# Kernel tuning notes

Hardware: AMD Instinct MI355X
Metric: run time of the kernel (lower is better)

## Reference

```python
import jax, jax.numpy as jnp
import numpy as np

RADIUS = 0.2
NSAMPLE = 32


def ball_query(new_xyz, xyz, radius, nsample):
    # new_xyz: (B, M, 3), xyz: (B, N, 3) -> idx: (B, M, nsample) int32
    B, M, _ = new_xyz.shape
    N = xyz.shape[1]
    # pairwise squared distances (B, M, N)
    diff = new_xyz[:, :, None, :] - xyz[:, None, :, :]
    dist2 = jnp.sum(diff * diff, axis=-1)
    mask = dist2 < (radius * radius)
    ar = jnp.arange(N, dtype=jnp.int32)
    masked = jnp.where(mask, ar[None, None, :], jnp.int32(N + 1))  # (B,M,N)
    sorted_idx = jnp.sort(masked, axis=2)[:, :, :nsample]          # (B,M,nsample)
    invalid = sorted_idx >= N
    first = sorted_idx[:, :, 0:1]
    idx = jnp.where(invalid, jnp.broadcast_to(first, sorted_idx.shape), sorted_idx)
    return idx


def group_points(points, idx):
    # points: (B, C, N), idx: (B, M, nsample) -> (B, C, M, nsample)
    B, C, N = points.shape
    M, ns = idx.shape[1], idx.shape[2]
    flat = jnp.broadcast_to(idx.reshape(B, 1, M * ns), (B, C, M * ns))
    return jnp.take_along_axis(points, flat, axis=2).reshape(B, C, M, ns)


def setup_inputs() -> dict:
    key = jax.random.key(0)
    k1, k2, k3 = jax.random.split(key, 3)
    xyz = jax.random.uniform(k1, (8, 16384, 3), dtype=jnp.float32)
    new_xyz = jax.random.uniform(k2, (8, 1024, 3), dtype=jnp.float32)
    features = jax.random.normal(k3, (8, 64, 16384), dtype=jnp.float32)
    return {"xyz": xyz, "new_xyz": new_xyz, "features": features}


def reference(xyz, new_xyz, features):
    idx = ball_query(new_xyz, xyz, RADIUS, NSAMPLE)          # (B,M,ns)
    xyz_t = jnp.transpose(xyz, (0, 2, 1))                    # (B,3,N)
    grouped_xyz = group_points(xyz_t, idx)                   # (B,3,M,ns)
    grouped_xyz = grouped_xyz - jnp.transpose(new_xyz, (0, 2, 1))[:, :, :, None]
    grouped_features = group_points(features, idx)           # (B,C,M,ns)
    new_features = jnp.concatenate([grouped_xyz, grouped_features], axis=1)
    return new_features                                      # (B, 3+C, M, ns)
```

## Files before the change

kernel.cpp:

```cpp
#include <hip/hip_runtime.h>


#define N_PTS   16384
#define M_Q     1024
#define B_SZ    8
#define NSAMP   32
#define NCH     64
#define R2      0.04f
#define OUT_CH  (3 + NCH)

__global__ __launch_bounds__(256) void transpose_kernel(
    const float* __restrict__ feat, float* __restrict__ ft)
{
    __shared__ float tile[64][65];
    const int b   = blockIdx.x >> 8;
    const int n0  = (blockIdx.x & 255) << 6;
    const int tid = threadIdx.x;
    const float* __restrict__ fb = feat + (size_t)b * NCH * N_PTS;
    float* __restrict__ tb       = ft   + ((size_t)b * N_PTS + n0) * NCH;

#pragma unroll
    for (int j = 0; j < 16; ++j) {
        const int idx = j * 256 + tid;
        const int c = idx >> 6, nn = idx & 63;
        tile[c][nn] = fb[(size_t)c * N_PTS + n0 + nn];
    }
    __syncthreads();
#pragma unroll
    for (int j = 0; j < 16; ++j) {
        const int idx = j * 256 + tid;
        const int nn = idx >> 6, cc = idx & 63;
        tb[(size_t)nn * NCH + cc] = tile[cc][nn];
    }
}

__global__ __launch_bounds__(128) void qg_main(
    const float* __restrict__ xyz,
    const float* __restrict__ new_xyz,
    const float* __restrict__ ft,
    float* __restrict__ out)
{
    const int tid  = threadIdx.x;
    const int w    = tid >> 6;
    const int lane = tid & 63;
    const int q    = blockIdx.x * 2 + w;
    const int b    = q >> 10;
    const int m    = q & (M_Q - 1);

    __shared__ int   idx_sh[2][NSAMP];
    __shared__ float tile[2][32][33];

    const float cx = new_xyz[q * 3 + 0];
    const float cy = new_xyz[q * 3 + 1];
    const float cz = new_xyz[q * 3 + 2];
    const float* __restrict__ xb = xyz + (size_t)b * N_PTS * 3;

    const unsigned long long lmask = (1ull << lane) - 1ull;
    int cnt = 0;
    for (int base = 0; base < N_PTS && cnt < NSAMP; base += 128) {
        const int nA = base + lane;
        const int nB = base + 64 + lane;
        const float ax = xb[nA * 3 + 0], ay = xb[nA * 3 + 1], az = xb[nA * 3 + 2];
        const float bx = xb[nB * 3 + 0], by = xb[nB * 3 + 1], bz = xb[nB * 3 + 2];

        {
            const float dx = __fsub_rn(cx, ax), dy = __fsub_rn(cy, ay), dz = __fsub_rn(cz, az);
            const float d2 = __fadd_rn(__fadd_rn(__fmul_rn(dx, dx), __fmul_rn(dy, dy)),
                                       __fmul_rn(dz, dz));
            const bool hit = d2 < R2;
            const unsigned long long mk = __ballot(hit);
            if (hit) {
                const int slot = cnt + __popcll(mk & lmask);
                if (slot < NSAMP) idx_sh[w][slot] = nA;
            }
            cnt += (int)__popcll(mk);
        }
        {
            const float dx = __fsub_rn(cx, bx), dy = __fsub_rn(cy, by), dz = __fsub_rn(cz, bz);
            const float d2 = __fadd_rn(__fadd_rn(__fmul_rn(dx, dx), __fmul_rn(dy, dy)),
                                       __fmul_rn(dz, dz));
            const bool hit = d2 < R2;
            const unsigned long long mk = __ballot(hit);
            if (hit) {
                const int slot = cnt + __popcll(mk & lmask);
                if (slot < NSAMP) idx_sh[w][slot] = nB;
            }
            cnt += (int)__popcll(mk);
        }
    }
    __syncthreads();

    if (lane < NSAMP) {
        const int v0 = (cnt > 0) ? idx_sh[w][0] : 0;
        if (lane >= cnt) idx_sh[w][lane] = v0;
    }
    __syncthreads();

    float* __restrict__ ob = out + ((size_t)b * OUT_CH * M_Q + (size_t)m) * NSAMP;
    for (int e = lane; e < 3 * NSAMP; e += 64) {
        const int c = e >> 5, s = e & 31;
        const int n = idx_sh[w][s];
        const float ctr = (c == 0) ? cx : ((c == 1) ? cy : cz);
        ob[(size_t)c * (M_Q * NSAMP) + s] = __fsub_rn(xb[n * 3 + c], ctr);
    }

    const float* __restrict__ ftb = ft + (size_t)b * N_PTS * NCH;
    const int sgrp = lane >> 3;
    const int c4   = lane & 7;

    for (int chunk = 0; chunk < 2; ++chunk) {
        float4 vals[4];
#pragma unroll
        for (int i = 0; i < 4; ++i) {
            const int s = i * 8 + sgrp;
            const int n = idx_sh[w][s];
            const float4* row = (const float4*)(ftb + (size_t)n * NCH + chunk * 32);
            vals[i] = row[c4];
        }
        __syncthreads();
#pragma unroll
        for (int i = 0; i < 4; ++i) {
            const int s = i * 8 + sgrp;
            tile[w][c4 * 4 + 0][s] = vals[i].x;
            tile[w][c4 * 4 + 1][s] = vals[i].y;
            tile[w][c4 * 4 + 2][s] = vals[i].z;
            tile[w][c4 * 4 + 3][s] = vals[i].w;
        }
        __syncthreads();
#pragma unroll
        for (int j = 0; j < 16; ++j) {
            const int idx = j * 64 + lane;
            const int c_local = idx >> 5;
            const int s = idx & 31;
            ob[(size_t)(3 + chunk * 32 + c_local) * (M_Q * NSAMP) + s] =
                tile[w][c_local][s];
        }
    }
}

__global__ __launch_bounds__(256) void qg_fallback(
    const float* __restrict__ xyz, const float* __restrict__ new_xyz,
    const float* __restrict__ feat, float* __restrict__ out)
{
    const int tid  = threadIdx.x;
    const int w    = tid >> 6;
    const int lane = tid & 63;
    const int q    = blockIdx.x * 4 + w;
    const int b    = q >> 10;
    const int m    = q & (M_Q - 1);

    __shared__ int idx_sh[4][NSAMP];

    const float cx = new_xyz[q * 3 + 0];
    const float cy = new_xyz[q * 3 + 1];
    const float cz = new_xyz[q * 3 + 2];
    const float* __restrict__ xb = xyz + (size_t)b * N_PTS * 3;

    int cnt = 0;
    for (int base = 0; base < N_PTS && cnt < NSAMP; base += 64) {
        const int n = base + lane;
        const float dx = __fsub_rn(cx, xb[n * 3 + 0]);
        const float dy = __fsub_rn(cy, xb[n * 3 + 1]);
        const float dz = __fsub_rn(cz, xb[n * 3 + 2]);
        const float d2 = __fadd_rn(__fadd_rn(__fmul_rn(dx, dx), __fmul_rn(dy, dy)),
                                   __fmul_rn(dz, dz));
        const bool hit = d2 < R2;
        const unsigned long long mk = __ballot(hit);
        if (hit) {
            const int slot = cnt + __popcll(mk & ((1ull << lane) - 1ull));
            if (slot < NSAMP) idx_sh[w][slot] = n;
        }
        cnt += (int)__popcll(mk);
    }
    __syncthreads();
    if (lane < NSAMP) {
        const int v0 = (cnt > 0) ? idx_sh[w][0] : 0;
        if (lane >= cnt) idx_sh[w][lane] = v0;
    }
    __syncthreads();

    const float* __restrict__ fb = feat + (size_t)b * NCH * N_PTS;
    float* __restrict__ ob = out + ((size_t)b * OUT_CH * M_Q + (size_t)m) * NSAMP;
    for (int e = lane; e < OUT_CH * NSAMP; e += 64) {
        const int c = e >> 5, s = e & 31;
        const int n = idx_sh[w][s];
        float v;
        if (c < 3) {
            const float ctr = (c == 0) ? cx : ((c == 1) ? cy : cz);
            v = __fsub_rn(xb[n * 3 + c], ctr);
        } else {
            v = fb[(size_t)(c - 3) * N_PTS + n];
        }
        ob[(size_t)c * (M_Q * NSAMP) + s] = v;
    }
}

extern "C" void kernel_launch(void* const* d_in, const int* in_sizes, int n_in,
                              void* d_out, int out_size, void* d_ws, size_t ws_size,
                              hipStream_t stream) {
    const float* xyz     = (const float*)d_in[0];
    const float* new_xyz = (const float*)d_in[1];
    const float* feat    = (const float*)d_in[2];
    float* out           = (float*)d_out;

    const size_t need = (size_t)B_SZ * N_PTS * NCH * sizeof(float);
    if (ws_size >= need) {
        transpose_kernel<<<B_SZ * (N_PTS / 64), 256, 0, stream>>>(feat, (float*)d_ws);
        qg_main<<<(B_SZ * M_Q) / 2, 128, 0, stream>>>(xyz, new_xyz, (const float*)d_ws, out);
    } else {
        qg_fallback<<<(B_SZ * M_Q) / 4, 256, 0, stream>>>(xyz, new_xyz, feat, out);
    }
}
```

Measured before the change: 140.8 us.

## Vectorize stores, prefetch xyz, cache neighbor coords in LDS, drop barriers

The transpose kernel now uses nontemporal loads, float4 stores and a batch-interleaved block order. The main kernel moves to 4 waves per block, also interleaved by batch. The ball-query loop software-prefetches the next 128 points, and each hit stores its coordinates and index in shared memory so the xyz output no longer re-gathers from global memory. Block-wide __syncthreads are removed because each wave only touches its own LDS slice, and outputs are written with vectorized nontemporal float4 stores. The risk is that without barriers, correctness depends on wave-local LDS ordering.

After: 143.4 us. About the same (+1.8%).

```diff
diff --git a/kernel.cpp b/kernel.cpp
--- a/kernel.cpp
+++ b/kernel.cpp
@@ -9,12 +9,14 @@
 #define R2      0.04f
 #define OUT_CH  (3 + NCH)
 
+typedef float f4 __attribute__((ext_vector_type(4)));
+
 __global__ __launch_bounds__(256) void transpose_kernel(
     const float* __restrict__ feat, float* __restrict__ ft)
 {
     __shared__ float tile[64][65];
-    const int b   = blockIdx.x >> 8;
-    const int n0  = (blockIdx.x & 255) << 6;
+    const int b   = blockIdx.x & 7;
+    const int n0  = (blockIdx.x >> 3) << 6;
     const int tid = threadIdx.x;
     const float* __restrict__ fb = feat + (size_t)b * NCH * N_PTS;
     float* __restrict__ tb       = ft   + ((size_t)b * N_PTS + n0) * NCH;
@@ -23,18 +25,24 @@
     for (int j = 0; j < 16; ++j) {
         const int idx = j * 256 + tid;
         const int c = idx >> 6, nn = idx & 63;
-        tile[c][nn] = fb[(size_t)c * N_PTS + n0 + nn];
+        tile[c][nn] = __builtin_nontemporal_load(&fb[(size_t)c * N_PTS + n0 + nn]);
     }
     __syncthreads();
-#pragma unroll
-    for (int j = 0; j < 16; ++j) {
-        const int idx = j * 256 + tid;
-        const int nn = idx >> 6, cc = idx & 63;
-        tb[(size_t)nn * NCH + cc] = tile[cc][nn];
-    }
-}
-
-__global__ __launch_bounds__(128) void qg_main(
+    const int c4 = tid & 15;
+    const int r  = tid >> 4;
+#pragma unroll
+    for (int j = 0; j < 4; ++j) {
+        const int nn = j * 16 + r;
+        f4 o;
+        o.x = tile[c4 * 4 + 0][nn];
+        o.y = tile[c4 * 4 + 1][nn];
+        o.z = tile[c4 * 4 + 2][nn];
+        o.w = tile[c4 * 4 + 3][nn];
+        *(f4*)(&tb[(size_t)nn * NCH + c4 * 4]) = o;
+    }
+}
+
+__global__ __launch_bounds__(256) void qg_main(
     const float* __restrict__ xyz,
     const float* __restrict__ new_xyz,
     const float* __restrict__ ft,
@@ -43,12 +51,12 @@
     const int tid  = threadIdx.x;
     const int w    = tid >> 6;
     const int lane = tid & 63;
-    const int q    = blockIdx.x * 2 + w;
-    const int b    = q >> 10;
-    const int m    = q & (M_Q - 1);
-
-    __shared__ int   idx_sh[2][NSAMP];
-    __shared__ float tile[2][32][33];
+    const int b    = blockIdx.x & 7;
+    const int m    = ((blockIdx.x >> 3) << 2) + w;
+    const int q    = (b << 10) + m;
+
+    __shared__ float pxyz[4][NSAMP][4];
+    __shared__ float tile[4][32][33];
 
     const float cx = new_xyz[q * 3 + 0];
     const float cy = new_xyz[q * 3 + 1];
@@ -57,67 +65,97 @@
 
     const unsigned long long lmask = (1ull << lane) - 1ull;
     int cnt = 0;
-    for (int base = 0; base < N_PTS && cnt < NSAMP; base += 128) {
-        const int nA = base + lane;
-        const int nB = base + 64 + lane;
-        const float ax = xb[nA * 3 + 0], ay = xb[nA * 3 + 1], az = xb[nA * 3 + 2];
-        const float bx = xb[nB * 3 + 0], by = xb[nB * 3 + 1], bz = xb[nB * 3 + 2];
+    float Ax = xb[lane * 3 + 0],        Ay = xb[lane * 3 + 1],        Az = xb[lane * 3 + 2];
+    float Bx = xb[(64 + lane) * 3 + 0], By = xb[(64 + lane) * 3 + 1], Bz = xb[(64 + lane) * 3 + 2];
+
+    for (int base = 0; ; base += 128) {
+        const int  nbase = base + 128;
+        const bool more  = nbase < N_PTS;
+        const int  pA = more ? nbase + lane : lane;
+        const int  pB = pA + 64;
+        const float nAx = xb[pA * 3 + 0], nAy = xb[pA * 3 + 1], nAz = xb[pA * 3 + 2];
+        const float nBx = xb[pB * 3 + 0], nBy = xb[pB * 3 + 1], nBz = xb[pB * 3 + 2];
 
         {
-            const float dx = __fsub_rn(cx, ax), dy = __fsub_rn(cy, ay), dz = __fsub_rn(cz, az);
+            const float dx = __fsub_rn(cx, Ax), dy = __fsub_rn(cy, Ay), dz = __fsub_rn(cz, Az);
             const float d2 = __fadd_rn(__fadd_rn(__fmul_rn(dx, dx), __fmul_rn(dy, dy)),
                                        __fmul_rn(dz, dz));
             const bool hit = d2 < R2;
             const unsigned long long mk = __ballot(hit);
             if (hit) {
                 const int slot = cnt + __popcll(mk & lmask);
-                if (slot < NSAMP) idx_sh[w][slot] = nA;
+                if (slot < NSAMP) {
+                    pxyz[w][slot][0] = Ax;
+                    pxyz[w][slot][1] = Ay;
+                    pxyz[w][slot][2] = Az;
+                    pxyz[w][slot][3] = __int_as_float(base + lane);
+                }
             }
             cnt += (int)__popcll(mk);
         }
         {
-            const float dx = __fsub_rn(cx, bx), dy = __fsub_rn(cy, by), dz = __fsub_rn(cz, bz);
+            const float dx = __fsub_rn(cx, Bx), dy = __fsub_rn(cy, By), dz = __fsub_rn(cz, Bz);
             const float d2 = __fadd_rn(__fadd_rn(__fmul_rn(dx, dx), __fmul_rn(dy, dy)),
                                        __fmul_rn(dz, dz));
             const bool hit = d2 < R2;
             const unsigned long long mk = __ballot(hit);
             if (hit) {
                 const int slot = cnt + __popcll(mk & lmask);
-                if (slot < NSAMP) idx_sh[w][slot] = nB;
+                if (slot < NSAMP) {
+                    pxyz[w][slot][0] = Bx;
+                    pxyz[w][slot][1] = By;
+                    pxyz[w][slot][2] = Bz;
+                    pxyz[w][slot][3] = __int_as_float(base + 64 + lane);
+                }
             }
             cnt += (int)__popcll(mk);
         }
-    }
-    __syncthreads();
-
-    if (lane < NSAMP) {
-        const int v0 = (cnt > 0) ? idx_sh[w][0] : 0;
-        if (lane >= cnt) idx_sh[w][lane] = v0;
-    }
-    __syncthreads();
+        if (cnt >= NSAMP || !more) break;
+        Ax = nAx; Ay = nAy; Az = nAz;
+        Bx = nBx; By = nBy; Bz = nBz;
+    }
+
+    if (lane < NSAMP && cnt < NSAMP) {
+        float v0x, v0y, v0z, v0w;
+        if (cnt > 0) {
+            v0x = pxyz[w][0][0]; v0y = pxyz[w][0][1];
+            v0z = pxyz[w][0][2]; v0w = pxyz[w][0][3];
+        } else {
+            v0x = xb[0]; v0y = xb[1]; v0z = xb[2]; v0w = __int_as_float(0);
+        }
+        if (lane >= cnt) {
+            pxyz[w][lane][0] = v0x; pxyz[w][lane][1] = v0y;
+            pxyz[w][lane][2] = v0z; pxyz[w][lane][3] = v0w;
+        }
+    }
 
     float* __restrict__ ob = out + ((size_t)b * OUT_CH * M_Q + (size_t)m) * NSAMP;
-    for (int e = lane; e < 3 * NSAMP; e += 64) {
-        const int c = e >> 5, s = e & 31;
-        const int n = idx_sh[w][s];
+
+    if (lane < 24) {
+        const int c  = lane >> 3;
+        const int s4 = lane & 7;
         const float ctr = (c == 0) ? cx : ((c == 1) ? cy : cz);
-        ob[(size_t)c * (M_Q * NSAMP) + s] = __fsub_rn(xb[n * 3 + c], ctr);
+        f4 o;
+        o.x = __fsub_rn(pxyz[w][s4 * 4 + 0][c], ctr);
+        o.y = __fsub_rn(pxyz[w][s4 * 4 + 1][c], ctr);
+        o.z = __fsub_rn(pxyz[w][s4 * 4 + 2][c], ctr);
+        o.w = __fsub_rn(pxyz[w][s4 * 4 + 3][c], ctr);
+        __builtin_nontemporal_store(o, (f4*)&ob[(size_t)c * (M_Q * NSAMP) + s4 * 4]);
     }
 
     const float* __restrict__ ftb = ft + (size_t)b * N_PTS * NCH;
     const int sgrp = lane >> 3;
     const int c4   = lane & 7;
 
+#pragma unroll
     for (int chunk = 0; chunk < 2; ++chunk) {
-        float4 vals[4];
+        f4 vals[4];
 #pragma unroll
         for (int i = 0; i < 4; ++i) {
             const int s = i * 8 + sgrp;
-            const int n = idx_sh[w][s];
-            const float4* row = (const float4*)(ftb + (size_t)n * NCH + chunk * 32);
-            vals[i] = row[c4];
-        }
-        __syncthreads();
+            const int n = __float_as_int(pxyz[w][s][3]);
+            vals[i] = *(const f4*)(ftb + (size_t)n * NCH + chunk * 32 + c4 * 4);
+        }
 #pragma unroll
         for (int i = 0; i < 4; ++i) {
             const int s = i * 8 + sgrp;
@@ -126,14 +164,17 @@
             tile[w][c4 * 4 + 2][s] = vals[i].z;
             tile[w][c4 * 4 + 3][s] = vals[i].w;
         }
-        __syncthreads();
-#pragma unroll
-        for (int j = 0; j < 16; ++j) {
-            const int idx = j * 64 + lane;
-            const int c_local = idx >> 5;
-            const int s = idx & 31;
-            ob[(size_t)(3 + chunk * 32 + c_local) * (M_Q * NSAMP) + s] =
-                tile[w][c_local][s];
+#pragma unroll
+        for (int j = 0; j < 4; ++j) {
+            const int c_loc = j * 8 + (lane >> 3);
+            const int s4    = lane & 7;
+            f4 o;
+            o.x = tile[w][c_loc][s4 * 4 + 0];
+            o.y = tile[w][c_loc][s4 * 4 + 1];
+            o.z = tile[w][c_loc][s4 * 4 + 2];
+            o.w = tile[w][c_loc][s4 * 4 + 3];
+            __builtin_nontemporal_store(
+                o, (f4*)&ob[(size_t)(3 + chunk * 32 + c_loc) * (M_Q * NSAMP) + s4 * 4]);
         }
     }
 }
@@ -206,7 +247,7 @@
     const size_t need = (size_t)B_SZ * N_PTS * NCH * sizeof(float);
     if (ws_size >= need) {
         transpose_kernel<<<B_SZ * (N_PTS / 64), 256, 0, stream>>>(feat, (float*)d_ws);
-        qg_main<<<(B_SZ * M_Q) / 2, 128, 0, stream>>>(xyz, new_xyz, (const float*)d_ws, out);
+        qg_main<<<(B_SZ * M_Q) / 4, 256, 0, stream>>>(xyz, new_xyz, (const float*)d_ws, out);
     } else {
         qg_fallback<<<(B_SZ * M_Q) / 4, 256, 0, stream>>>(xyz, new_xyz, feat, out);
     }
```
